# Kernel optimization log

Measured on AMD Instinct MI355X. Metric: run time of the kernel, lower is better.

Reference implementation:

```python
import jax, jax.numpy as jnp
import numpy as np

H = 32       # total query heads
HK = 8       # kv heads (GQA)
D = 128      # head_dim = hidden // H
HIDDEN = 4096
THETA = 10000.0


def setup_inputs() -> dict:
    key = jax.random.key(0)
    k1, k2, k3 = jax.random.split(key, 3)
    B, S = 2, 2048
    positions = jnp.arange(S, dtype=jnp.int32)
    hidden_states = jax.random.normal(k1, (B, S, HIDDEN), dtype=jnp.float32)
    w_qkv = jax.random.normal(k2, (HIDDEN, (H + 2 * HK) * D), dtype=jnp.float32) * 0.02
    w_o = jax.random.normal(k3, (H * D, HIDDEN), dtype=jnp.float32) * 0.02
    return {"positions": positions, "hidden_states": hidden_states,
            "w_qkv": w_qkv, "w_o": w_o}


def _rope(x, cos, sin):
    # neox-style rotary: split halves, rotate
    x1, x2 = jnp.split(x, 2, axis=-1)
    return jnp.concatenate([x1 * cos - x2 * sin, x2 * cos + x1 * sin], axis=-1)


def reference(positions, hidden_states, w_qkv, w_o):
    B, S, _ = hidden_states.shape
    qkv = hidden_states @ w_qkv                        # [B,S,(H+2HK)*D]
    q, k, v = jnp.split(qkv, [H * D, H * D + HK * D], axis=-1)
    q = q.reshape(B, S, H, D)
    k = k.reshape(B, S, HK, D)
    v = v.reshape(B, S, HK, D)

    inv_freq = 1.0 / (THETA ** (jnp.arange(0, D, 2, dtype=jnp.float32) / D))
    freqs = positions.astype(jnp.float32)[:, None] * inv_freq[None, :]  # [S,D/2]
    cos = jnp.cos(freqs)[None, :, None, :]
    sin = jnp.sin(freqs)[None, :, None, :]
    q = _rope(q, cos, sin)
    k = _rope(k, cos, sin)

    G = H // HK  # query heads per kv head
    qg = q.reshape(B, S, HK, G, D)
    scores = jnp.einsum('bqhgd,bkhd->bhgqk', qg, k) * (D ** -0.5)
    causal = jnp.tril(jnp.ones((S, S), dtype=bool))
    scores = jnp.where(causal[None, None, None], scores, jnp.float32(-1e30))
    probs = jax.nn.softmax(scores, axis=-1)
    out = jnp.einsum('bhgqk,bkhd->bqhgd', probs, v).reshape(B, S, H * D)
    return out @ w_o
```

## Files before the change

### kernel.cpp

```cpp
#include <hip/hip_runtime.h>

typedef unsigned short ushort_t;
typedef __attribute__((ext_vector_type(8))) short short8;
typedef __attribute__((ext_vector_type(4))) unsigned short ushort4_t;
typedef __attribute__((ext_vector_type(4))) float f32x4;

#define NH 32
#define NHK 8
#define HD 128
#define HID 4096
#define NB 2
#define SEQ 2048
#define NQKV ((NH + 2 * NHK) * HD)

static __device__ inline ushort_t f2bu(float x) {
  unsigned u = __builtin_bit_cast(unsigned, x);
  unsigned r = (u + 0x7FFFu + ((u >> 16) & 1u)) >> 16;
  return (ushort_t)r;
}

typedef __attribute__((address_space(1))) void gvoid;
typedef __attribute__((address_space(3))) void lvoid;
static __device__ inline void gld16(const void* g, void* l) {
  __builtin_amdgcn_global_load_lds((gvoid*)g, (lvoid*)l, 16, 0, 0);
}

__global__ void rope_tab_k(const int* __restrict__ positions, float* __restrict__ tab) {
  int i = blockIdx.x * 256 + threadIdx.x;
  int s = i >> 6, d = i & 63;
  float pos = (float)positions[s];
  float f = pos * exp2f(-0.20762050593046014f * (float)d);
  tab[2 * i] = cosf(f);
  tab[2 * i + 1] = sinf(f);
}

__global__ void h2b_k(const float* __restrict__ in, ushort_t* __restrict__ out) {
  long i = ((long)blockIdx.x * 256 + threadIdx.x) * 8;
  f32x4 a = *(const f32x4*)&in[i];
  f32x4 b = *(const f32x4*)&in[i + 4];
  ushort4_t ya, yb;
#pragma unroll
  for (int u = 0; u < 4; ++u) { ya[u] = f2bu(a[u]); yb[u] = f2bu(b[u]); }
  *(ushort4_t*)&out[i] = ya;
  *(ushort4_t*)&out[i + 4] = yb;
}

__global__ void wt_k(const float* __restrict__ in, ushort_t* __restrict__ out,
                     int K, int N) {
  __shared__ ushort_t T[64][72];
  int n0 = blockIdx.x * 64, k0 = blockIdx.y * 64;
  int t = threadIdx.x;
  int kr = t >> 4, nc = (t & 15) * 4;
#pragma unroll
  for (int p = 0; p < 4; ++p) {
    int k = kr + p * 16;
    f32x4 x = *(const f32x4*)&in[(long)(k0 + k) * N + n0 + nc];
    ushort4_t y;
#pragma unroll
    for (int u = 0; u < 4; ++u) y[u] = f2bu(x[u]);
    *(ushort4_t*)&T[k][nc] = y;
  }
  __syncthreads();
  int n = t >> 2, kc = (t & 3) * 16;
  ushort_t tmp[16];
#pragma unroll
  for (int j = 0; j < 16; ++j) tmp[j] = T[kc + j][n];
  *(short8*)&out[(long)(n0 + n) * K + k0 + kc] = *(short8*)&tmp[0];
  *(short8*)&out[(long)(n0 + n) * K + k0 + kc + 8] = *(short8*)&tmp[8];
}

template <int MODE>
__global__ __attribute__((amdgpu_flat_work_group_size(256, 256),
                          amdgpu_waves_per_eu(2, 2)))
void gemm_bt(const ushort_t* __restrict__ A,
             const ushort_t* __restrict__ Bt,
             float* __restrict__ C,
             const float* __restrict__ tab,
             ushort_t* __restrict__ Qo,
             ushort_t* __restrict__ Ko,
             ushort_t* __restrict__ Vo,
             int M, int N, int K) {
  __shared__ ushort_t As[128 * 32];
  __shared__ ushort_t Bs[128 * 32];
  int m0 = blockIdx.y * 128, n0 = blockIdx.x * 128;
  int tid = threadIdx.x;
  int lane = tid & 63, wave = tid >> 6;
  int wm = wave * 32;
  int l15 = lane & 15, quad = lane >> 4;
  f32x4 acc[2][8];
#pragma unroll
  for (int i = 0; i < 2; ++i)
#pragma unroll
    for (int j = 0; j < 8; ++j) acc[i][j] = (f32x4){0.f, 0.f, 0.f, 0.f};

  int iw = wave * 2;
  for (int k0 = 0; k0 < K; k0 += 32) {
    __syncthreads();
#pragma unroll
    for (int ii = 0; ii < 2; ++ii) {
      int i = iw + ii;
      int row = i * 16 + (lane >> 2);
      int gk = ((lane & 3) ^ ((row >> 1) & 3)) * 8;
      gld16(&A[(long)(m0 + row) * K + k0 + gk], &As[i * 512]);
      gld16(&Bt[(long)(n0 + row) * K + k0 + gk], &Bs[i * 512]);
    }
    __syncthreads();
    short8 af[2], bfr[8];
#pragma unroll
    for (int i = 0; i < 2; ++i) {
      int r = wm + i * 16 + l15;
      af[i] = *(short8*)&As[r * 32 + ((quad ^ ((r >> 1) & 3)) << 3)];
    }
#pragma unroll
    for (int j = 0; j < 8; ++j) {
      int r = j * 16 + l15;
      bfr[j] = *(short8*)&Bs[r * 32 + ((quad ^ ((r >> 1) & 3)) << 3)];
    }
#pragma unroll
    for (int i = 0; i < 2; ++i)
#pragma unroll
      for (int j = 0; j < 8; ++j)
        acc[i][j] = __builtin_amdgcn_mfma_f32_16x16x32_bf16(af[i], bfr[j], acc[i][j], 0, 0, 0);
  }

  if (MODE == 0) {
#pragma unroll
    for (int i = 0; i < 2; ++i)
#pragma unroll
      for (int j = 0; j < 8; ++j)
#pragma unroll
        for (int r = 0; r < 4; ++r) {
          int row = m0 + wm + i * 16 + quad * 4 + r;
          int col = n0 + j * 16 + l15;
          C[(long)row * N + col] = acc[i][j][r];
        }
  } else {
    int head = n0 >> 7;
    const float2* tb = (const float2*)tab;
    if (head < NH + NHK) {
      bool isq = head < NH;
      ushort_t* dst = isq ? (Qo + (long)head * SEQ * HD)
                          : (Ko + (long)(head - NH) * SEQ * HD);
      float sc = isq ? 0.08838834764831845f : 1.0f;
#pragma unroll
      for (int i = 0; i < 2; ++i)
#pragma unroll
        for (int r = 0; r < 4; ++r) {
          int s = m0 + wm + i * 16 + quad * 4 + r;
#pragma unroll
          for (int j = 0; j < 4; ++j) {
            int d = j * 16 + l15;
            float2 cs = tb[s * 64 + d];
            float x1 = acc[i][j][r], x2 = acc[i][j + 4][r];
            dst[(long)s * HD + d] = f2bu((x1 * cs.x - x2 * cs.y) * sc);
            dst[(long)s * HD + d + 64] = f2bu((x2 * cs.x + x1 * cs.y) * sc);
          }
        }
    } else {
      int hk = head - NH - NHK;
      ushort_t* dst = Vo + (long)hk * HD * SEQ;
#pragma unroll
      for (int i = 0; i < 2; ++i)
#pragma unroll
        for (int j = 0; j < 8; ++j)
#pragma unroll
          for (int r = 0; r < 4; ++r) {
            int s = m0 + wm + i * 16 + quad * 4 + r;
            int d = j * 16 + l15;
            dst[(long)d * SEQ + s] = f2bu(acc[i][j][r]);
          }
    }
  }
}

template <int MODE, typename TA>
__global__ __attribute__((amdgpu_flat_work_group_size(256, 256),
                          amdgpu_waves_per_eu(2, 2)))
void gemm_kn(const TA* __restrict__ A,
             const float* __restrict__ B,
             float* __restrict__ C,
             const float* __restrict__ tab,
             ushort_t* __restrict__ Qo,
             ushort_t* __restrict__ Ko,
             ushort_t* __restrict__ Vo,
             int M, int N, int K) {
  __shared__ ushort_t As[128][40];
  __shared__ ushort_t Bs[128 * 32];
  int m0 = blockIdx.y * 128, n0 = blockIdx.x * 128;
  int tid = threadIdx.x;
  int lane = tid & 63, wave = tid >> 6;
  int wm = wave * 32;
  int l15 = lane & 15, quad = lane >> 4;
  f32x4 acc[2][8];
#pragma unroll
  for (int i = 0; i < 2; ++i)
#pragma unroll
    for (int j = 0; j < 8; ++j) acc[i][j] = (f32x4){0.f, 0.f, 0.f, 0.f};

  for (int k0 = 0; k0 < K; k0 += 32) {
    __syncthreads();
    if constexpr (sizeof(TA) == 2) {
#pragma unroll
      for (int it = 0; it < 2; ++it) {
        int v = tid + it * 256;
        int row = v >> 2, kc = (v & 3) * 8;
        *(short8*)&As[row][kc] =
            *(const short8*)&A[(long)(m0 + row) * K + k0 + kc];
      }
    } else {
#pragma unroll
      for (int it = 0; it < 4; ++it) {
        int v = tid + it * 256;
        int row = v >> 3, kc = (v & 7) * 4;
        f32x4 x = *(const f32x4*)&A[(long)(m0 + row) * K + k0 + kc];
        ushort4_t y;
#pragma unroll
        for (int u = 0; u < 4; ++u) y[u] = f2bu(x[u]);
        *(ushort4_t*)&As[row][kc] = y;
      }
    }
#pragma unroll
    for (int it = 0; it < 4; ++it) {
      int v = tid + it * 256;
      int kr = v >> 5, nc = (v & 31) * 4;
      f32x4 x = *(const f32x4*)&B[(long)(k0 + kr) * N + n0 + nc];
      int kg = (kr >> 3) << 3, ke = kr & 7;
#pragma unroll
      for (int u = 0; u < 4; ++u) {
        int n = nc + u;
        Bs[n * 32 + ((kg ^ (((n >> 2) & 3) << 3))) + ke] = f2bu(x[u]);
      }
    }
    __syncthreads();
    short8 af[2], bfr[8];
#pragma unroll
    for (int i = 0; i < 2; ++i) af[i] = *(short8*)&As[wm + i * 16 + l15][quad * 8];
#pragma unroll
    for (int j = 0; j < 8; ++j) {
      int n = j * 16 + l15;
      bfr[j] = *(short8*)&Bs[n * 32 + ((quad ^ ((n >> 2) & 3)) << 3)];
    }
#pragma unroll
    for (int i = 0; i < 2; ++i)
#pragma unroll
      for (int j = 0; j < 8; ++j)
        acc[i][j] = __builtin_amdgcn_mfma_f32_16x16x32_bf16(af[i], bfr[j], acc[i][j], 0, 0, 0);
  }

  if (MODE == 0) {
#pragma unroll
    for (int i = 0; i < 2; ++i)
#pragma unroll
      for (int j = 0; j < 8; ++j)
#pragma unroll
        for (int r = 0; r < 4; ++r) {
          int row = m0 + wm + i * 16 + quad * 4 + r;
          int col = n0 + j * 16 + l15;
          C[(long)row * N + col] = acc[i][j][r];
        }
  } else {
    int head = n0 >> 7;
    const float2* tb = (const float2*)tab;
    if (head < NH + NHK) {
      bool isq = head < NH;
      ushort_t* dst = isq ? (Qo + (long)head * SEQ * HD)
                          : (Ko + (long)(head - NH) * SEQ * HD);
      float sc = isq ? 0.08838834764831845f : 1.0f;
#pragma unroll
      for (int i = 0; i < 2; ++i)
#pragma unroll
        for (int r = 0; r < 4; ++r) {
          int s = m0 + wm + i * 16 + quad * 4 + r;
#pragma unroll
          for (int j = 0; j < 4; ++j) {
            int d = j * 16 + l15;
            float2 cs = tb[s * 64 + d];
            float x1 = acc[i][j][r], x2 = acc[i][j + 4][r];
            dst[(long)s * HD + d] = f2bu((x1 * cs.x - x2 * cs.y) * sc);
            dst[(long)s * HD + d + 64] = f2bu((x2 * cs.x + x1 * cs.y) * sc);
          }
        }
    } else {
      int hk = head - NH - NHK;
      ushort_t* dst = Vo + (long)hk * HD * SEQ;
#pragma unroll
      for (int i = 0; i < 2; ++i)
#pragma unroll
        for (int j = 0; j < 8; ++j)
#pragma unroll
          for (int r = 0; r < 4; ++r) {
            int s = m0 + wm + i * 16 + quad * 4 + r;
            int d = j * 16 + l15;
            dst[(long)d * SEQ + s] = f2bu(acc[i][j][r]);
          }
    }
  }
}

__global__ __launch_bounds__(256, 2) void attn_k(const ushort_t* __restrict__ Q,
                                                 const ushort_t* __restrict__ Kg,
                                                 const ushort_t* __restrict__ Vt,
                                                 ushort_t* __restrict__ Aout) {
  __shared__ ushort_t Ks[32][136];
  __shared__ ushort_t Vs[128][40];
  __shared__ ushort_t Ps[4][16][32];
  int qt = blockIdx.x * 64;
  int h = blockIdx.y;
  int hk = h >> 2;
  const ushort_t* Qh = Q + (long)h * SEQ * HD;
  const ushort_t* Kh = Kg + (long)hk * SEQ * HD;
  const ushort_t* Vh = Vt + (long)hk * HD * SEQ;
  int tid = threadIdx.x, lane = tid & 63, wave = tid >> 6;
  int l15 = lane & 15, quad = lane >> 4;
  int qw = qt + wave * 16;
  short8 qf[4];
#pragma unroll
  for (int c = 0; c < 4; ++c)
    qf[c] = *(const short8*)&Qh[(long)(qw + l15) * HD + c * 32 + quad * 8];
  f32x4 O[8];
#pragma unroll
  for (int dt = 0; dt < 8; ++dt) O[dt] = (f32x4){0.f, 0.f, 0.f, 0.f};
  float mrow[4], lrow[4];
#pragma unroll
  for (int r = 0; r < 4; ++r) { mrow[r] = -1e30f; lrow[r] = 0.f; }
  int kend = qt + 64;
  for (int kc = 0; kc < kend; kc += 32) {
    __syncthreads();
#pragma unroll
    for (int i = 0; i < 2; ++i) {
      int v = tid + i * 256;
      int kr = v >> 4, dc = (v & 15) * 8;
      *(short8*)&Ks[kr][dc] = *(const short8*)&Kh[(long)(kc + kr) * HD + dc];
    }
#pragma unroll
    for (int i = 0; i < 2; ++i) {
      int v = tid + i * 256;
      int dr = v >> 2, kcol = (v & 3) * 8;
      *(short8*)&Vs[dr][kcol] = *(const short8*)&Vh[(long)dr * SEQ + kc + kcol];
    }
    __syncthreads();
    bool active = (kc <= qw + 15);
    if (active) {
      f32x4 S0 = (f32x4){0.f, 0.f, 0.f, 0.f}, S1 = (f32x4){0.f, 0.f, 0.f, 0.f};
#pragma unroll
      for (int c = 0; c < 4; ++c) {
        short8 kf0 = *(short8*)&Ks[l15][c * 32 + quad * 8];
        short8 kf1 = *(short8*)&Ks[16 + l15][c * 32 + quad * 8];
        S0 = __builtin_amdgcn_mfma_f32_16x16x32_bf16(qf[c], kf0, S0, 0, 0, 0);
        S1 = __builtin_amdgcn_mfma_f32_16x16x32_bf16(qf[c], kf1, S1, 0, 0, 0);
      }
#pragma unroll
      for (int r = 0; r < 4; ++r) {
        int qrow = qw + quad * 4 + r;
        float v0 = (kc + l15 <= qrow) ? S0[r] : -1e30f;
        float v1 = (kc + 16 + l15 <= qrow) ? S1[r] : -1e30f;
        float mx = fmaxf(v0, v1);
        mx = fmaxf(mx, __shfl_xor(mx, 1, 64));
        mx = fmaxf(mx, __shfl_xor(mx, 2, 64));
        mx = fmaxf(mx, __shfl_xor(mx, 4, 64));
        mx = fmaxf(mx, __shfl_xor(mx, 8, 64));
        float mnew = fmaxf(mrow[r], mx);
        float alpha = __expf(mrow[r] - mnew);
        float p0 = __expf(v0 - mnew);
        float p1 = __expf(v1 - mnew);
        float rs = p0 + p1;
        rs += __shfl_xor(rs, 1, 64);
        rs += __shfl_xor(rs, 2, 64);
        rs += __shfl_xor(rs, 4, 64);
        rs += __shfl_xor(rs, 8, 64);
        lrow[r] = lrow[r] * alpha + rs;
        mrow[r] = mnew;
#pragma unroll
        for (int dt = 0; dt < 8; ++dt) O[dt][r] *= alpha;
        Ps[wave][quad * 4 + r][l15] = f2bu(p0);
        Ps[wave][quad * 4 + r][16 + l15] = f2bu(p1);
      }
    }
    __syncthreads();
    if (active) {
      short8 pf = *(short8*)&Ps[wave][l15][quad * 8];
#pragma unroll
      for (int dt = 0; dt < 8; ++dt) {
        short8 vf = *(short8*)&Vs[dt * 16 + l15][quad * 8];
        O[dt] = __builtin_amdgcn_mfma_f32_16x16x32_bf16(pf, vf, O[dt], 0, 0, 0);
      }
    }
  }
#pragma unroll
  for (int dt = 0; dt < 8; ++dt)
#pragma unroll
    for (int r = 0; r < 4; ++r) {
      int q = qw + quad * 4 + r;
      float o = O[dt][r] / lrow[r];
      Aout[(long)q * (NH * HD) + h * HD + dt * 16 + l15] = f2bu(o);
    }
}

extern "C" void kernel_launch(void* const* d_in, const int* in_sizes, int n_in,
                              void* d_out, int out_size, void* d_ws, size_t ws_size,
                              hipStream_t stream) {
  const int* positions = (const int*)d_in[0];
  const float* hidden = (const float*)d_in[1];
  const float* w_qkv = (const float*)d_in[2];
  const float* w_o = (const float*)d_in[3];
  char* ws = (char*)d_ws;
  ushort_t* Qb = (ushort_t*)(ws + 0L);
  ushort_t* Kb = (ushort_t*)(ws + 16777216L);
  ushort_t* Vtb = (ushort_t*)(ws + 20971520L);
  ushort_t* attno = (ushort_t*)(ws + 25165824L);
  float* tab = (float*)attno;
  ushort_t* hb16 = (ushort_t*)(ws + 41943040L);
  ushort_t* wqkvT = (ushort_t*)(ws + 75497472L);
  ushort_t* woT = (ushort_t*)(ws + 125829120L);
  float* outf = (float*)d_out;
  bool big = ws_size >= 159383552ULL;

  if (big) {
    h2b_k<<<dim3((NB * SEQ * HID) / (256 * 8)), 256, 0, stream>>>(hidden, hb16);
    wt_k<<<dim3(NQKV / 64, HID / 64), 256, 0, stream>>>(w_qkv, wqkvT, HID, NQKV);
    wt_k<<<dim3(HID / 64, HID / 64), 256, 0, stream>>>(w_o, woT, HID, HID);
  }
  for (int b = 0; b < NB; ++b) {
    rope_tab_k<<<dim3((SEQ * 64) / 256), 256, 0, stream>>>(positions, tab);
    if (big) {
      gemm_bt<1><<<dim3(NQKV / 128, SEQ / 128), 256, 0, stream>>>(
          hb16 + (long)b * SEQ * HID, wqkvT, nullptr, tab, Qb, Kb, Vtb,
          SEQ, NQKV, HID);
    } else {
      gemm_kn<1, float><<<dim3(NQKV / 128, SEQ / 128), 256, 0, stream>>>(
          hidden + (long)b * SEQ * HID, w_qkv, nullptr, tab, Qb, Kb, Vtb,
          SEQ, NQKV, HID);
    }
    attn_k<<<dim3(SEQ / 64, NH), 256, 0, stream>>>(Qb, Kb, Vtb, attno);
    if (big) {
      gemm_bt<0><<<dim3(HID / 128, SEQ / 128), 256, 0, stream>>>(
          attno, woT, outf + (long)b * SEQ * HID, nullptr, nullptr, nullptr,
          nullptr, SEQ, HID, HID);
    } else {
      gemm_kn<0, ushort_t><<<dim3(HID / 128, SEQ / 128), 256, 0, stream>>>(
          attno, w_o, outf + (long)b * SEQ * HID, nullptr, nullptr, nullptr,
          nullptr, SEQ, HID, HID);
    }
  }
}
```

Baseline: 1.243 ms.

## Double attention KV tile to 64 keys and launch heaviest causal blocks first

```diff
diff --git a/kernel.cpp b/kernel.cpp
--- a/kernel.cpp
+++ b/kernel.cpp
@@ -301,10 +301,10 @@
                                                  const ushort_t* __restrict__ Kg,
                                                  const ushort_t* __restrict__ Vt,
                                                  ushort_t* __restrict__ Aout) {
-  __shared__ ushort_t Ks[32][136];
-  __shared__ ushort_t Vs[128][40];
-  __shared__ ushort_t Ps[4][16][32];
-  int qt = blockIdx.x * 64;
+  __shared__ ushort_t Ks[64][136];
+  __shared__ ushort_t Vs[128][72];
+  __shared__ ushort_t Ps[4][16][72];
+  int qt = ((int)gridDim.x - 1 - blockIdx.x) * 64;
   int h = blockIdx.y;
   int hk = h >> 2;
   const ushort_t* Qh = Q + (long)h * SEQ * HD;
@@ -324,46 +324,52 @@
 #pragma unroll
   for (int r = 0; r < 4; ++r) { mrow[r] = -1e30f; lrow[r] = 0.f; }
   int kend = qt + 64;
-  for (int kc = 0; kc < kend; kc += 32) {
-    __syncthreads();
-#pragma unroll
-    for (int i = 0; i < 2; ++i) {
+  for (int kc = 0; kc < kend; kc += 64) {
+    __syncthreads();
+#pragma unroll
+    for (int i = 0; i < 4; ++i) {
       int v = tid + i * 256;
       int kr = v >> 4, dc = (v & 15) * 8;
       *(short8*)&Ks[kr][dc] = *(const short8*)&Kh[(long)(kc + kr) * HD + dc];
     }
 #pragma unroll
-    for (int i = 0; i < 2; ++i) {
+    for (int i = 0; i < 4; ++i) {
       int v = tid + i * 256;
-      int dr = v >> 2, kcol = (v & 3) * 8;
+      int dr = v >> 3, kcol = (v & 7) * 8;
       *(short8*)&Vs[dr][kcol] = *(const short8*)&Vh[(long)dr * SEQ + kc + kcol];
     }
     __syncthreads();
     bool active = (kc <= qw + 15);
     if (active) {
-      f32x4 S0 = (f32x4){0.f, 0.f, 0.f, 0.f}, S1 = (f32x4){0.f, 0.f, 0.f, 0.f};
+      f32x4 S[4];
+#pragma unroll
+      for (int t = 0; t < 4; ++t) S[t] = (f32x4){0.f, 0.f, 0.f, 0.f};
 #pragma unroll
       for (int c = 0; c < 4; ++c) {
-        short8 kf0 = *(short8*)&Ks[l15][c * 32 + quad * 8];
-        short8 kf1 = *(short8*)&Ks[16 + l15][c * 32 + quad * 8];
-        S0 = __builtin_amdgcn_mfma_f32_16x16x32_bf16(qf[c], kf0, S0, 0, 0, 0);
-        S1 = __builtin_amdgcn_mfma_f32_16x16x32_bf16(qf[c], kf1, S1, 0, 0, 0);
+#pragma unroll
+        for (int t = 0; t < 4; ++t) {
+          short8 kf = *(short8*)&Ks[t * 16 + l15][c * 32 + quad * 8];
+          S[t] = __builtin_amdgcn_mfma_f32_16x16x32_bf16(qf[c], kf, S[t], 0, 0, 0);
+        }
       }
 #pragma unroll
       for (int r = 0; r < 4; ++r) {
         int qrow = qw + quad * 4 + r;
-        float v0 = (kc + l15 <= qrow) ? S0[r] : -1e30f;
-        float v1 = (kc + 16 + l15 <= qrow) ? S1[r] : -1e30f;
-        float mx = fmaxf(v0, v1);
+        float vv[4];
+#pragma unroll
+        for (int t = 0; t < 4; ++t)
+          vv[t] = (kc + t * 16 + l15 <= qrow) ? S[t][r] : -1e30f;
+        float mx = fmaxf(fmaxf(vv[0], vv[1]), fmaxf(vv[2], vv[3]));
         mx = fmaxf(mx, __shfl_xor(mx, 1, 64));
         mx = fmaxf(mx, __shfl_xor(mx, 2, 64));
         mx = fmaxf(mx, __shfl_xor(mx, 4, 64));
         mx = fmaxf(mx, __shfl_xor(mx, 8, 64));
         float mnew = fmaxf(mrow[r], mx);
         float alpha = __expf(mrow[r] - mnew);
-        float p0 = __expf(v0 - mnew);
-        float p1 = __expf(v1 - mnew);
-        float rs = p0 + p1;
+        float p[4];
+#pragma unroll
+        for (int t = 0; t < 4; ++t) p[t] = __expf(vv[t] - mnew);
+        float rs = (p[0] + p[1]) + (p[2] + p[3]);
         rs += __shfl_xor(rs, 1, 64);
         rs += __shfl_xor(rs, 2, 64);
         rs += __shfl_xor(rs, 4, 64);
@@ -372,17 +378,21 @@
         mrow[r] = mnew;
 #pragma unroll
         for (int dt = 0; dt < 8; ++dt) O[dt][r] *= alpha;
-        Ps[wave][quad * 4 + r][l15] = f2bu(p0);
-        Ps[wave][quad * 4 + r][16 + l15] = f2bu(p1);
+#pragma unroll
+        for (int t = 0; t < 4; ++t)
+          Ps[wave][quad * 4 + r][t * 16 + l15] = f2bu(p[t]);
       }
     }
     __syncthreads();
     if (active) {
-      short8 pf = *(short8*)&Ps[wave][l15][quad * 8];
+      short8 pf0 = *(short8*)&Ps[wave][l15][quad * 8];
+      short8 pf1 = *(short8*)&Ps[wave][l15][32 + quad * 8];
 #pragma unroll
       for (int dt = 0; dt < 8; ++dt) {
-        short8 vf = *(short8*)&Vs[dt * 16 + l15][quad * 8];
-        O[dt] = __builtin_amdgcn_mfma_f32_16x16x32_bf16(pf, vf, O[dt], 0, 0, 0);
+        short8 vf0 = *(short8*)&Vs[dt * 16 + l15][quad * 8];
+        short8 vf1 = *(short8*)&Vs[dt * 16 + l15][32 + quad * 8];
+        O[dt] = __builtin_amdgcn_mfma_f32_16x16x32_bf16(pf0, vf0, O[dt], 0, 0, 0);
+        O[dt] = __builtin_amdgcn_mfma_f32_16x16x32_bf16(pf1, vf1, O[dt], 0, 0, 0);
       }
     }
   }
```

Measured after the change: 1.158 ms. 1.07x faster.
